# Optimization experiments

Measured on AMD Instinct MI355X. Metric: run time of the kernel, lower is better.

Reference implementation:

```python
import jax, jax.numpy as jnp
import numpy as np

NUM_HEADS = 8
HEAD_DIM = 128
ATTN_SCALE = 0.12


def _rope_tables(T, head_dim, dtype=jnp.float32):
    # half-truncate RoPE from modded-nanogpt: base-freq bounded, half the dims unrotated
    angular_freq = (1.0 / 1024.0) ** jnp.linspace(0.0, 1.0, head_dim // 4, dtype=dtype)
    angular_freq = jnp.concatenate([angular_freq, jnp.zeros(head_dim // 4, dtype=dtype)])  # [D/2]
    t = jnp.arange(T, dtype=dtype)
    theta = t[:, None] * angular_freq[None, :]  # [T, D/2]
    return jnp.cos(theta), jnp.sin(theta)


def _apply_rope(x, cos, sin):
    # x: [B, T, H, D]; cos/sin: [T, D/2]
    x1, x2 = jnp.split(x, 2, axis=-1)
    c = cos[None, :, None, :]
    s = sin[None, :, None, :]
    y1 = x1 * c + x2 * s
    y2 = x2 * c - x1 * s
    return jnp.concatenate([y1, y2], axis=-1)


def _rms_norm(x):
    eps = jnp.asarray(jnp.finfo(x.dtype).eps, x.dtype)
    var = jnp.mean(jnp.square(x), axis=-1, keepdims=True)
    return x * jax.lax.rsqrt(var + eps)


def setup_inputs() -> dict:
    key = jax.random.key(0)
    ks = jax.random.split(key, 4)
    B, T, dim = 1, 4096, 1024
    hdim = NUM_HEADS * HEAD_DIM
    std = 0.5 * dim ** (-0.5)
    bound = (3.0 ** 0.5) * std
    x = jax.random.normal(ks[0], (B, T, dim), dtype=jnp.float32)
    ve = jax.random.normal(ks[1], (B, T, hdim), dtype=jnp.float32)
    qkv_w = jax.random.uniform(ks[2], (3, hdim, dim), dtype=jnp.float32, minval=-bound, maxval=bound)
    lambdas = jnp.array([0.5, 0.5], dtype=jnp.float32)
    c_proj_w = jax.random.normal(ks[3], (dim, hdim), dtype=jnp.float32) * 0.02
    return {"x": x, "ve": ve, "qkv_w": qkv_w, "lambdas": lambdas, "c_proj_w": c_proj_w}


def reference(x, ve, qkv_w, lambdas, c_proj_w):
    B, T, dim = x.shape
    H, D = NUM_HEADS, HEAD_DIM
    # fused QKV projection: qkv_w is [3, H*D, dim]
    w = qkv_w.reshape(3 * H * D, dim)
    qkv = jnp.einsum('btd,fd->btf', x, w).reshape(B, T, 3, H, D)
    q, k, v = qkv[:, :, 0], qkv[:, :, 1], qkv[:, :, 2]  # each [B, T, H, D]
    q = _rms_norm(q)
    k = _rms_norm(k)
    cos, sin = _rope_tables(T, D, dtype=jnp.float32)
    q = _apply_rope(q, cos, sin)
    k = _apply_rope(k, cos, sin)
    # lambda-weighted value blend with value embeddings
    v = lambdas[0] * v + lambdas[1] * ve.reshape(B, T, H, D)
    # causal attention, scale = 0.12
    scores = jnp.einsum('bthd,bshd->bhts', q, k) * ATTN_SCALE  # [B, H, T, T]
    causal = jnp.tril(jnp.ones((T, T), dtype=bool))
    scores = jnp.where(causal[None, None, :, :], scores, jnp.asarray(-jnp.inf, scores.dtype))
    p = jax.nn.softmax(scores, axis=-1)
    y = jnp.einsum('bhts,bshd->bthd', p, v).reshape(B, T, H * D)
    return jnp.einsum('btf,df->btd', y, c_proj_w)
```

## Files before the change

kernel.cpp:

```cpp
#include <hip/hip_runtime.h>
#include <hip/hip_bf16.h>

typedef __attribute__((ext_vector_type(4))) float f32x4;
typedef __attribute__((ext_vector_type(16))) float f32x16;
typedef __attribute__((ext_vector_type(8))) __bf16 bf16x8;
typedef unsigned short u16;
typedef unsigned int u32;
typedef __attribute__((ext_vector_type(4))) u16 u16x4;

__device__ __forceinline__ u16 f2bf(float f) {
    u32 u = __builtin_bit_cast(u32, f);
    u32 r = (u + 0x7FFFu + ((u >> 16) & 1u)) >> 16;
    return (u16)r;
}
__device__ __forceinline__ float bf2f(u16 h) {
    return __builtin_bit_cast(float, ((u32)h) << 16);
}
__device__ __forceinline__ bf16x8 ld_frag(const u16* p) {
    uint4 v = *reinterpret_cast<const uint4*>(p);
    return __builtin_bit_cast(bf16x8, v);
}
__device__ __forceinline__ void gld_lds(const u16* gp, u16* lp) {
    __builtin_amdgcn_global_load_lds(
        (const __attribute__((address_space(1))) u32*)gp,
        (__attribute__((address_space(3))) u32*)lp, 16, 0, 0);
}
__device__ __forceinline__ u32 pk_bf16(float lo, float hi) {
    u32 r;
    asm("v_cvt_pk_bf16_f32 %0, %1, %2" : "=v"(r) : "v"(lo), "v"(hi));
    return r;
}
__device__ __forceinline__ void unp8(uint4 v, float* f) {
    f[0] = bf2f((u16)(v.x & 0xffffu)); f[1] = bf2f((u16)(v.x >> 16));
    f[2] = bf2f((u16)(v.y & 0xffffu)); f[3] = bf2f((u16)(v.y >> 16));
    f[4] = bf2f((u16)(v.z & 0xffffu)); f[5] = bf2f((u16)(v.z >> 16));
    f[6] = bf2f((u16)(v.w & 0xffffu)); f[7] = bf2f((u16)(v.w >> 16));
}

__global__ __launch_bounds__(256) void cvt3(const float* __restrict__ x,
                                            const float* __restrict__ w,
                                            const float* __restrict__ c,
                                            u16* __restrict__ xb,
                                            u16* __restrict__ wb,
                                            u16* __restrict__ cb) {
    int b = blockIdx.x;
    const float* in;
    u16* out;
    int i;
    if (b < 4096)      { in = x; out = xb; i = b * 256 + threadIdx.x; }
    else if (b < 7168) { in = w; out = wb; i = (b - 4096) * 256 + threadIdx.x; }
    else               { in = c; out = cb; i = (b - 7168) * 256 + threadIdx.x; }
    float4 v = reinterpret_cast<const float4*>(in)[i];
    u16x4 o;
    o.x = f2bf(v.x); o.y = f2bf(v.y); o.z = f2bf(v.z); o.w = f2bf(v.w);
    *reinterpret_cast<u16x4*>(out + 4 * (size_t)i) = o;
}

__global__ __launch_bounds__(256) void rope_tab(float* __restrict__ ctab,
                                                float* __restrict__ stab) {
    int i = blockIdx.x * 256 + threadIdx.x;
    int t = i >> 6, j = i & 63;
    float c = 1.0f, s = 0.0f;
    if (j < 32) {
        float f = exp2f(-10.0f * (float)j / 31.0f);
        float th = (float)t * f;
        c = cosf(th); s = sinf(th);
    }
    ctab[i] = c; stab[i] = s;
}

__global__ __launch_bounds__(256, 6) void gemm_qkv(const u16* __restrict__ A,
                                                   const u16* __restrict__ B,
                                                   const float* __restrict__ ve,
                                                   const float* __restrict__ lambdas,
                                                   const float* __restrict__ ctab,
                                                   const float* __restrict__ stab,
                                                   u16* __restrict__ Qb,
                                                   u16* __restrict__ Kb,
                                                   u16* __restrict__ Vt) {
    __shared__ u16 smem[12288];
    const int K = 1024;
    const int tid = threadIdx.x;
    const int w = tid >> 6, l = tid & 63;
    const int bid = blockIdx.x;
    const int bm = bid & 63, bn = bid >> 6;
    const int g = l >> 4, c16 = l & 15;
    const int wr = w >> 1, wc = w & 1;

    f32x4 acc[2][4] = {};

    auto stage = [&](int bi, int kt) {
        {
            int r = w * 16 + (l >> 2);
            int gs = (l & 3) ^ ((r >> 1) & 3);
            gld_lds(A + (size_t)(bm * 64 + r) * K + kt * 32 + gs * 8,
                    smem + bi * 2048 + w * 512);
        }
#pragma unroll
        for (int cc = 0; cc < 2; ++cc) {
            int c = 2 * w + cc;
            int r = 16 * c + (l >> 2);
            int gs = (l & 3) ^ ((r >> 1) & 3);
            gld_lds(B + (size_t)(bn * 128 + r) * K + kt * 32 + gs * 8,
                    smem + 4096 + bi * 4096 + c * 512);
        }
    };

    const int NT = K >> 5;
    stage(0, 0);
    __syncthreads();
    for (int kt = 0; kt < NT; ++kt) {
        int cur = kt & 1;
        if (kt + 1 < NT) stage(cur ^ 1, kt + 1);
        bf16x8 af[2], bf[4];
#pragma unroll
        for (int mi = 0; mi < 2; ++mi) {
            int r = wr * 32 + mi * 16 + c16;
            int sl = g ^ ((r >> 1) & 3);
            af[mi] = ld_frag(smem + cur * 2048 + r * 32 + sl * 8);
        }
#pragma unroll
        for (int ni = 0; ni < 4; ++ni) {
            int r = wc * 64 + ni * 16 + c16;
            int sl = g ^ ((r >> 1) & 3);
            bf[ni] = ld_frag(smem + 4096 + cur * 4096 + r * 32 + sl * 8);
        }
#pragma unroll
        for (int mi = 0; mi < 2; ++mi)
#pragma unroll
            for (int ni = 0; ni < 4; ++ni)
                acc[mi][ni] = __builtin_amdgcn_mfma_f32_16x16x32_bf16(
                    af[mi], bf[ni], acc[mi][ni], 0, 0, 0);
        __syncthreads();
    }

    const int which = bn >> 3, h = bn & 7;
    if (which < 2) {
#pragma unroll
        for (int mi = 0; mi < 2; ++mi)
#pragma unroll
            for (int ni = 0; ni < 4; ++ni) {
                int col = wc * 64 + ni * 16 + c16;
                int row0 = wr * 32 + mi * 16 + g * 4;
#pragma unroll
                for (int r = 0; r < 4; ++r)
                    smem[(row0 + r) * 136 + col] = f2bf(acc[mi][ni][r]);
            }
        __syncthreads();
        const int row = tid >> 2, p = tid & 3;
        const int t = bm * 64 + row;
        const u16* src = smem + row * 136;
        const int j0 = p * 16;
        float x1[16], x2[16];
#pragma unroll
        for (int e = 0; e < 16; e += 8) {
            unp8(*(const uint4*)(src + j0 + e), x1 + e);
            unp8(*(const uint4*)(src + 64 + j0 + e), x2 + e);
        }
        float ss = 0.0f;
#pragma unroll
        for (int e = 0; e < 16; ++e) ss += x1[e] * x1[e] + x2[e] * x2[e];
        ss += __shfl_xor(ss, 1);
        ss += __shfl_xor(ss, 2);
        float rs = rsqrtf(ss * (1.0f / 128.0f) + 1.1920929e-07f);
        if (which == 0) rs *= 0.12f;
        u16* dst = (which ? Kb : Qb) + ((size_t)h * 4096 + t) * 128;
        u16 o1[16], o2[16];
#pragma unroll
        for (int e = 0; e < 16; ++e) {
            int j = j0 + e;
            float c = ctab[t * 64 + j], s = stab[t * 64 + j];
            float a = x1[e] * rs, b = x2[e] * rs;
            o1[e] = f2bf(a * c + b * s);
            o2[e] = f2bf(b * c - a * s);
        }
#pragma unroll
        for (int e = 0; e < 16; e += 4) {
            *(u16x4*)(dst + j0 + e) = *(u16x4*)(o1 + e);
            *(u16x4*)(dst + 64 + j0 + e) = *(u16x4*)(o2 + e);
        }
    } else {
        const float l0 = lambdas[0], l1 = lambdas[1];
#pragma unroll
        for (int mi = 0; mi < 2; ++mi)
#pragma unroll
            for (int ni = 0; ni < 4; ++ni) {
                int col = wc * 64 + ni * 16 + c16;
                int row0 = wr * 32 + mi * 16 + g * 4;
#pragma unroll
                for (int r = 0; r < 4; ++r) {
                    int row = row0 + r;
                    float vv = l0 * acc[mi][ni][r]
                             + l1 * ve[(size_t)(bm * 64 + row) * 1024 + h * 128 + col];
                    int cp = (row & 51) | ((row & 4) << 1) | ((row & 8) >> 1);
                    smem[col * 72 + cp] = f2bf(vv);
                }
            }
        __syncthreads();
        const int d = tid >> 1, seg = tid & 1;
        const u16* lsrc = smem + d * 72 + seg * 32;
        u16* gdst = Vt + ((size_t)h * 128 + d) * 4096 + bm * 64 + seg * 32;
#pragma unroll
        for (int q2 = 0; q2 < 4; ++q2)
            *(uint4*)(gdst + q2 * 8) = *(const uint4*)(lsrc + q2 * 8);
    }
}

__global__ __launch_bounds__(256) void gemm_nt_f32(const u16* __restrict__ A,
                                                   const u16* __restrict__ B,
                                                   float* __restrict__ Cout,
                                                   int M, int N, int K, int ldc) {
    __shared__ u16 smem[8192];
    const int tid = threadIdx.x;
    const int w = tid >> 6, l = tid & 63;
    const int bm = blockIdx.x & 63, bn = blockIdx.x >> 6;
    const int g = l >> 4, c16 = l & 15;
    const int wr = w >> 1, wc = w & 1;

    f32x4 acc[2][2] = {};

    auto stage = [&](int bi, int kt) {
        {
            int r = w * 16 + (l >> 2);
            int gs = (l & 3) ^ ((r >> 1) & 3);
            gld_lds(A + (size_t)(bm * 64 + r) * K + kt * 32 + gs * 8,
                    smem + bi * 2048 + w * 512);
        }
        {
            int r = w * 16 + (l >> 2);
            int gs = (l & 3) ^ ((r >> 1) & 3);
            gld_lds(B + (size_t)(bn * 64 + r) * K + kt * 32 + gs * 8,
                    smem + 4096 + bi * 2048 + w * 512);
        }
    };

    const int NT = K >> 5;
    stage(0, 0);
    __syncthreads();
    for (int kt = 0; kt < NT; ++kt) {
        int cur = kt & 1;
        if (kt + 1 < NT) stage(cur ^ 1, kt + 1);
        bf16x8 af[2], bf[2];
#pragma unroll
        for (int mi = 0; mi < 2; ++mi) {
            int r = wr * 32 + mi * 16 + c16;
            int sl = g ^ ((r >> 1) & 3);
            af[mi] = ld_frag(smem + cur * 2048 + r * 32 + sl * 8);
        }
#pragma unroll
        for (int ni = 0; ni < 2; ++ni) {
            int r = wc * 32 + ni * 16 + c16;
            int sl = g ^ ((r >> 1) & 3);
            bf[ni] = ld_frag(smem + 4096 + cur * 2048 + r * 32 + sl * 8);
        }
#pragma unroll
        for (int mi = 0; mi < 2; ++mi)
#pragma unroll
            for (int ni = 0; ni < 2; ++ni)
                acc[mi][ni] = __builtin_amdgcn_mfma_f32_16x16x32_bf16(
                    af[mi], bf[ni], acc[mi][ni], 0, 0, 0);
        __syncthreads();
    }
#pragma unroll
    for (int mi = 0; mi < 2; ++mi) {
#pragma unroll
        for (int ni = 0; ni < 2; ++ni) {
            int col = bn * 64 + wc * 32 + ni * 16 + c16;
            int row0 = bm * 64 + wr * 32 + mi * 16 + g * 4;
#pragma unroll
            for (int r = 0; r < 4; ++r)
                Cout[(size_t)(row0 + r) * ldc + col] = acc[mi][ni][r];
        }
    }
}

#define OPHALF 4194304
__global__ __launch_bounds__(256) void attn(const u16* __restrict__ Qb,
                                            const u16* __restrict__ Kb,
                                            const u16* __restrict__ Vt,
                                            u16* __restrict__ Op,
                                            float* __restrict__ ssumP) {
    __shared__ u16 smem[3 * 8192];
    const int bid = blockIdx.x;
    const int h = bid & 7;
    const int pid = bid >> 3;
    const int j = pid >> 1;
    const int half = pid & 1;
    const int tid = threadIdx.x;
    const int w = tid >> 6, l = tid & 63;
    const int qh = w & 1, kvh = w >> 1;
    const int l31 = l & 31, hi = l >> 5;
    const int krow = kvh * 32 + l31;

    for (int seg = 0; seg < 2; ++seg) {
        const int qb = seg ? (63 - j) : j;
        const int part = seg ? (1 - half) : half;
        const int s = (qb + 1) >> 1;
        const int t0 = part ? s : 0;
        const int t1 = part ? (qb + 1) : s;
        const int qg = qb * 64 + qh * 32 + l31;

        bf16x8 qf[8];
        {
            const u16* qp = Qb + ((size_t)h * 4096 + qg) * 128;
#pragma unroll
            for (int dk = 0; dk < 8; ++dk) qf[dk] = ld_frag(qp + dk * 16 + hi * 8);
        }

        const u16* kp[4];
        const u16* vp[4];
#pragma unroll
        for (int cc = 0; cc < 4; ++cc) {
            int c = 4 * w + cc;
            int rK = 4 * c + (l >> 4);
            int gsK = (l & 15) ^ (rK & 7);
            kp[cc] = Kb + ((size_t)h * 4096 + t0 * 64 + rK) * 128 + gsK * 8;
            int rV = 8 * c + (l >> 3);
            int gsV = (l & 7) ^ (rV & 7);
            vp[cc] = Vt + ((size_t)h * 128 + rV) * 4096 + t0 * 64 + gsV * 8;
        }

        f32x16 o[4] = {};
        float ssum = 0.0f;

        if (t0 < t1) {
#pragma unroll
            for (int cc = 0; cc < 4; ++cc) {
                gld_lds(kp[cc], smem + (4 * w + cc) * 512);
                kp[cc] += 8192;
            }
            __syncthreads();

            int cur = 0;
            for (int t = t0; t < t1; ++t) {
                if (t + 1 < t1) {
#pragma unroll
                    for (int cc = 0; cc < 4; ++cc) {
                        gld_lds(kp[cc], smem + (cur ^ 1) * 8192 + (4 * w + cc) * 512);
                        kp[cc] += 8192;
                    }
                }
#pragma unroll
                for (int cc = 0; cc < 4; ++cc) {
                    gld_lds(vp[cc], smem + 16384 + (4 * w + cc) * 512);
                    vp[cc] += 64;
                }

                const u16* sKc = smem + cur * 8192;
                f32x16 st = {};
                __builtin_amdgcn_s_setprio(1);
#pragma unroll
                for (int dk = 0; dk < 8; ++dk) {
                    int sl = (2 * dk + hi) ^ (krow & 7);
                    bf16x8 kf = ld_frag(sKc + krow * 128 + sl * 8);
                    st = __builtin_amdgcn_mfma_f32_32x32x16_bf16(kf, qf[dk], st, 0, 0, 0);
                }
                __builtin_amdgcn_s_setprio(0);

                float pv[16];
                if (t == qb) {
#pragma unroll
                    for (int r = 0; r < 16; ++r) {
                        int kvg = t * 64 + kvh * 32 + (r & 3) + 8 * (r >> 2) + 4 * hi;
                        pv[r] = (kvg <= qg) ? __expf(st[r]) : 0.0f;
                    }
                } else {
#pragma unroll
                    for (int r = 0; r < 16; ++r) pv[r] = __expf(st[r]);
                }
                float ps = 0.0f;
#pragma unroll
                for (int i = 0; i < 16; ++i) ps += pv[i];
                ssum += ps;

                bf16x8 pb[2];
#pragma unroll
                for (int m = 0; m < 2; ++m) {
                    uint4 u;
                    u.x = pk_bf16(pv[8 * m + 0], pv[8 * m + 1]);
                    u.y = pk_bf16(pv[8 * m + 2], pv[8 * m + 3]);
                    u.z = pk_bf16(pv[8 * m + 4], pv[8 * m + 5]);
                    u.w = pk_bf16(pv[8 * m + 6], pv[8 * m + 7]);
                    pb[m] = __builtin_bit_cast(bf16x8, u);
                }

                __syncthreads();

                const u16* sVc = smem + 16384;
                __builtin_amdgcn_s_setprio(1);
#pragma unroll
                for (int m = 0; m < 2; ++m) {
#pragma unroll
                    for (int dt = 0; dt < 4; ++dt) {
                        int drow = dt * 32 + l31;
                        int sl = (4 * kvh + 2 * m + hi) ^ (drow & 7);
                        bf16x8 vf = ld_frag(sVc + drow * 64 + sl * 8);
                        o[dt] = __builtin_amdgcn_mfma_f32_32x32x16_bf16(vf, pb[m], o[dt], 0, 0, 0);
                    }
                }
                __builtin_amdgcn_s_setprio(0);
                __syncthreads();
                cur ^= 1;
            }
        } else {
            __syncthreads();
        }

        ssum += __shfl_xor(ssum, 32);

        float* sO = (float*)smem;
        float* sS = (float*)smem + 8448;
        if (kvh == 1) {
            float* base = sO + (qh * 32 + l31) * 132;
#pragma unroll
            for (int dt = 0; dt < 4; ++dt)
#pragma unroll
                for (int i = 0; i < 4; ++i) {
                    int d0 = dt * 32 + i * 8 + hi * 4;
                    float4 v = {o[dt][4 * i + 0], o[dt][4 * i + 1],
                                o[dt][4 * i + 2], o[dt][4 * i + 3]};
                    *(float4*)(base + d0) = v;
                }
            if (hi == 0) sS[qh * 32 + l31] = ssum;
        }
        __syncthreads();
        if (kvh == 0) {
            float stot = ssum + sS[qh * 32 + l31];
            const float* base = sO + (qh * 32 + l31) * 132;
            u16* orow = Op + (size_t)part * OPHALF + ((size_t)(h * 4096 + qg)) * 128;
#pragma unroll
            for (int dt = 0; dt < 4; ++dt)
#pragma unroll
                for (int i = 0; i < 4; ++i) {
                    int d0 = dt * 32 + i * 8 + hi * 4;
                    float4 prev = *(const float4*)(base + d0);
                    u16x4 ov;
                    ov.x = f2bf(o[dt][4 * i + 0] + prev.x);
                    ov.y = f2bf(o[dt][4 * i + 1] + prev.y);
                    ov.z = f2bf(o[dt][4 * i + 2] + prev.z);
                    ov.w = f2bf(o[dt][4 * i + 3] + prev.w);
                    *(u16x4*)(orow + d0) = ov;
                }
            if (hi == 0) ssumP[part * 32768 + h * 4096 + qg] = stot;
        }
        __syncthreads();
    }
}

__global__ __launch_bounds__(256) void combine(const u16* __restrict__ Op,
                                               const float* __restrict__ ssumP,
                                               u16* __restrict__ Y) {
    int i = blockIdx.x * 256 + threadIdx.x;
    int d4 = i & 31;
    int hq = i >> 5;
    int h = hq >> 12, q = hq & 4095;
    u16x4 a = ((const u16x4*)Op)[i];
    u16x4 b = ((const u16x4*)(Op + OPHALF))[i];
    float inv = 1.0f / (ssumP[hq] + ssumP[32768 + hq]);
    u16x4 ov;
    ov.x = f2bf((bf2f(a.x) + bf2f(b.x)) * inv);
    ov.y = f2bf((bf2f(a.y) + bf2f(b.y)) * inv);
    ov.z = f2bf((bf2f(a.z) + bf2f(b.z)) * inv);
    ov.w = f2bf((bf2f(a.w) + bf2f(b.w)) * inv);
    *(u16x4*)(Y + (size_t)q * 1024 + h * 128 + d4 * 4) = ov;
}

extern "C" void kernel_launch(void* const* d_in, const int* in_sizes, int n_in,
                              void* d_out, int out_size, void* d_ws, size_t ws_size,
                              hipStream_t stream) {
    const float* x = (const float*)d_in[0];
    const float* ve = (const float*)d_in[1];
    const float* qkv_w = (const float*)d_in[2];
    const float* lambdas = (const float*)d_in[3];
    const float* c_proj_w = (const float*)d_in[4];

    char* ws = (char*)d_ws;
    size_t o = 0;
    u16* qkvb = (u16*)(ws + o); o += (size_t)4096 * 3072 * 2;
    u16* xb   = (u16*)(ws + o); o += (size_t)4096 * 1024 * 2;
    u16* wb   = (u16*)(ws + o); o += (size_t)3072 * 1024 * 2;
    u16* cb   = (u16*)(ws + o); o += (size_t)1024 * 1024 * 2;
    u16* Qb   = (u16*)(ws + o); o += (size_t)8 * 4096 * 128 * 2;
    u16* Kb   = (u16*)(ws + o); o += (size_t)8 * 4096 * 128 * 2;
    u16* Vt   = (u16*)(ws + o); o += (size_t)8 * 4096 * 128 * 2;
    u16* Yb   = (u16*)(ws + o); o += (size_t)4096 * 1024 * 2;
    float* ctab = (float*)(ws + o); o += (size_t)4096 * 64 * 4;
    float* stab = (float*)(ws + o); o += (size_t)4096 * 64 * 4;
    u16* Op      = qkvb;
    float* ssumP = (float*)wb;

    cvt3<<<8192, 256, 0, stream>>>(x, qkv_w, c_proj_w, xb, wb, cb);
    rope_tab<<<1024, 256, 0, stream>>>(ctab, stab);
    gemm_qkv<<<64 * 24, 256, 0, stream>>>(xb, wb, ve, lambdas, ctab, stab, Qb, Kb, Vt);
    attn<<<512, 256, 0, stream>>>(Qb, Kb, Vt, Op, ssumP);
    combine<<<4096, 256, 0, stream>>>(Op, ssumP, Yb);
    gemm_nt_f32<<<64 * 16, 256, 0, stream>>>(Yb, cb, (float*)d_out, 4096, 1024, 1024, 1024);
}
```

Measured before the change: 137.3 us.

## Process two 64-row query blocks per attention block to reuse K/V tiles

Each attention workgroup now handles a 128-row query tile as two 64-row sub-tiles that share every K and V tile loaded into LDS. This halves global-to-LDS K/V traffic and barrier count per query row, and roughly doubles MFMA work per sync. The causal work split is rebalanced to 32 query tiles with a new midpoint split, and the kernel gets a launch-bounds occupancy hint of 2. It costs many more registers (two Q fragment sets, two score and output accumulators), which may limit occupancy. The grid launch is presumably changed outside the shown lines.

```diff
diff --git a/kernel.cpp b/kernel.cpp
--- a/kernel.cpp
+++ b/kernel.cpp
@@ -275,11 +275,11 @@
 }
 
 #define OPHALF 4194304
-__global__ __launch_bounds__(256) void attn(const u16* __restrict__ Qb,
-                                            const u16* __restrict__ Kb,
-                                            const u16* __restrict__ Vt,
-                                            u16* __restrict__ Op,
-                                            float* __restrict__ ssumP) {
+__global__ __launch_bounds__(256, 2) void attn(const u16* __restrict__ Qb,
+                                               const u16* __restrict__ Kb,
+                                               const u16* __restrict__ Vt,
+                                               u16* __restrict__ Op,
+                                               float* __restrict__ ssumP) {
     __shared__ u16 smem[3 * 8192];
     const int bid = blockIdx.x;
     const int h = bid & 7;
@@ -293,157 +293,168 @@
     const int krow = kvh * 32 + l31;
 
     for (int seg = 0; seg < 2; ++seg) {
-        const int qb = seg ? (63 - j) : j;
+        const int qb = seg ? (31 - j) : j;
         const int part = seg ? (1 - half) : half;
-        const int s = (qb + 1) >> 1;
+        const int s = qb + 1;
         const int t0 = part ? s : 0;
-        const int t1 = part ? (qb + 1) : s;
-        const int qg = qb * 64 + qh * 32 + l31;
-
-        bf16x8 qf[8];
-        {
-            const u16* qp = Qb + ((size_t)h * 4096 + qg) * 128;
-#pragma unroll
-            for (int dk = 0; dk < 8; ++dk) qf[dk] = ld_frag(qp + dk * 16 + hi * 8);
+        const int t1 = part ? (2 * qb + 2) : s;
+        const int qg0 = qb * 128 + qh * 32 + l31;
+        const int qg1 = qg0 + 64;
+
+        bf16x8 qf[2][8];
+#pragma unroll
+        for (int u = 0; u < 2; ++u) {
+            const u16* qp = Qb + ((size_t)h * 4096 + (u ? qg1 : qg0)) * 128;
+#pragma unroll
+            for (int dk = 0; dk < 8; ++dk) qf[u][dk] = ld_frag(qp + dk * 16 + hi * 8);
         }
 
         const u16* kp[4];
-        const u16* vp[4];
+        const u16* vp0;
 #pragma unroll
         for (int cc = 0; cc < 4; ++cc) {
             int c = 4 * w + cc;
             int rK = 4 * c + (l >> 4);
             int gsK = (l & 15) ^ (rK & 7);
             kp[cc] = Kb + ((size_t)h * 4096 + t0 * 64 + rK) * 128 + gsK * 8;
-            int rV = 8 * c + (l >> 3);
-            int gsV = (l & 7) ^ (rV & 7);
-            vp[cc] = Vt + ((size_t)h * 128 + rV) * 4096 + t0 * 64 + gsV * 8;
-        }
-
-        f32x16 o[4] = {};
-        float ssum = 0.0f;
-
-        if (t0 < t1) {
-#pragma unroll
-            for (int cc = 0; cc < 4; ++cc) {
-                gld_lds(kp[cc], smem + (4 * w + cc) * 512);
-                kp[cc] += 8192;
-            }
-            __syncthreads();
-
-            int cur = 0;
-            for (int t = t0; t < t1; ++t) {
-                if (t + 1 < t1) {
-#pragma unroll
-                    for (int cc = 0; cc < 4; ++cc) {
-                        gld_lds(kp[cc], smem + (cur ^ 1) * 8192 + (4 * w + cc) * 512);
-                        kp[cc] += 8192;
-                    }
+        }
+        {
+            int rV = 8 * (4 * w) + (l >> 3);
+            int gsV = (l & 7) ^ ((l >> 3) & 7);
+            vp0 = Vt + ((size_t)h * 128 + rV) * 4096 + t0 * 64 + gsV * 8;
+        }
+
+        f32x16 o[2][4] = {};
+        float ssum[2] = {0.0f, 0.0f};
+
+#pragma unroll
+        for (int cc = 0; cc < 4; ++cc) {
+            gld_lds(kp[cc], smem + (4 * w + cc) * 512);
+            kp[cc] += 8192;
+        }
+        __syncthreads();
+
+        int cur = 0;
+        for (int t = t0; t < t1; ++t) {
+            if (t + 1 < t1) {
+#pragma unroll
+                for (int cc = 0; cc < 4; ++cc) {
+                    gld_lds(kp[cc], smem + (cur ^ 1) * 8192 + (4 * w + cc) * 512);
+                    kp[cc] += 8192;
                 }
-#pragma unroll
-                for (int cc = 0; cc < 4; ++cc) {
-                    gld_lds(vp[cc], smem + 16384 + (4 * w + cc) * 512);
-                    vp[cc] += 64;
-                }
-
-                const u16* sKc = smem + cur * 8192;
-                f32x16 st = {};
-                __builtin_amdgcn_s_setprio(1);
-#pragma unroll
-                for (int dk = 0; dk < 8; ++dk) {
-                    int sl = (2 * dk + hi) ^ (krow & 7);
-                    bf16x8 kf = ld_frag(sKc + krow * 128 + sl * 8);
-                    st = __builtin_amdgcn_mfma_f32_32x32x16_bf16(kf, qf[dk], st, 0, 0, 0);
-                }
-                __builtin_amdgcn_s_setprio(0);
-
+            }
+#pragma unroll
+            for (int cc = 0; cc < 4; ++cc)
+                gld_lds(vp0 + (size_t)cc * 8 * 4096, smem + 16384 + (4 * w + cc) * 512);
+            vp0 += 64;
+
+            const u16* sKc = smem + cur * 8192;
+            f32x16 st0 = {}, st1 = {};
+            __builtin_amdgcn_s_setprio(1);
+#pragma unroll
+            for (int dk = 0; dk < 8; ++dk) {
+                int sl = (2 * dk + hi) ^ (krow & 7);
+                bf16x8 kf = ld_frag(sKc + krow * 128 + sl * 8);
+                st0 = __builtin_amdgcn_mfma_f32_32x32x16_bf16(kf, qf[0][dk], st0, 0, 0, 0);
+                st1 = __builtin_amdgcn_mfma_f32_32x32x16_bf16(kf, qf[1][dk], st1, 0, 0, 0);
+            }
+            __builtin_amdgcn_s_setprio(0);
+
+            bf16x8 pb[2][2];
+#pragma unroll
+            for (int u = 0; u < 2; ++u) {
+                f32x16 stv = u ? st1 : st0;
+                const int qg = u ? qg1 : qg0;
+                const int qmin = qb * 128 + u * 64 + qh * 32;
                 float pv[16];
-                if (t == qb) {
+                if (t * 64 + 63 > qmin) {
 #pragma unroll
                     for (int r = 0; r < 16; ++r) {
                         int kvg = t * 64 + kvh * 32 + (r & 3) + 8 * (r >> 2) + 4 * hi;
-                        pv[r] = (kvg <= qg) ? __expf(st[r]) : 0.0f;
+                        pv[r] = (kvg <= qg) ? __expf(stv[r]) : 0.0f;
                     }
                 } else {
 #pragma unroll
-                    for (int r = 0; r < 16; ++r) pv[r] = __expf(st[r]);
+                    for (int r = 0; r < 16; ++r) pv[r] = __expf(stv[r]);
                 }
                 float ps = 0.0f;
 #pragma unroll
                 for (int i = 0; i < 16; ++i) ps += pv[i];
-                ssum += ps;
-
-                bf16x8 pb[2];
+                ssum[u] += ps;
 #pragma unroll
                 for (int m = 0; m < 2; ++m) {
-                    uint4 u;
-                    u.x = pk_bf16(pv[8 * m + 0], pv[8 * m + 1]);
-                    u.y = pk_bf16(pv[8 * m + 2], pv[8 * m + 3]);
-                    u.z = pk_bf16(pv[8 * m + 4], pv[8 * m + 5]);
-                    u.w = pk_bf16(pv[8 * m + 6], pv[8 * m + 7]);
-                    pb[m] = __builtin_bit_cast(bf16x8, u);
+                    uint4 uu;
+                    uu.x = pk_bf16(pv[8 * m + 0], pv[8 * m + 1]);
+                    uu.y = pk_bf16(pv[8 * m + 2], pv[8 * m + 3]);
+                    uu.z = pk_bf16(pv[8 * m + 4], pv[8 * m + 5]);
+                    uu.w = pk_bf16(pv[8 * m + 6], pv[8 * m + 7]);
+                    pb[u][m] = __builtin_bit_cast(bf16x8, uu);
                 }
-
-                __syncthreads();
-
-                const u16* sVc = smem + 16384;
-                __builtin_amdgcn_s_setprio(1);
-#pragma unroll
-                for (int m = 0; m < 2; ++m) {
-#pragma unroll
-                    for (int dt = 0; dt < 4; ++dt) {
-                        int drow = dt * 32 + l31;
-                        int sl = (4 * kvh + 2 * m + hi) ^ (drow & 7);
-                        bf16x8 vf = ld_frag(sVc + drow * 64 + sl * 8);
-                        o[dt] = __builtin_amdgcn_mfma_f32_32x32x16_bf16(vf, pb[m], o[dt], 0, 0, 0);
-                    }
+            }
+
+            __syncthreads();
+
+            const u16* sVc = smem + 16384;
+            __builtin_amdgcn_s_setprio(1);
+#pragma unroll
+            for (int m = 0; m < 2; ++m) {
+#pragma unroll
+                for (int dt = 0; dt < 4; ++dt) {
+                    int drow = dt * 32 + l31;
+                    int sl = (4 * kvh + 2 * m + hi) ^ (drow & 7);
+                    bf16x8 vf = ld_frag(sVc + drow * 64 + sl * 8);
+                    o[0][dt] = __builtin_amdgcn_mfma_f32_32x32x16_bf16(vf, pb[0][m], o[0][dt], 0, 0, 0);
+                    o[1][dt] = __builtin_amdgcn_mfma_f32_32x32x16_bf16(vf, pb[1][m], o[1][dt], 0, 0, 0);
                 }
-                __builtin_amdgcn_s_setprio(0);
-                __syncthreads();
-                cur ^= 1;
-            }
-        } else {
+            }
+            __builtin_amdgcn_s_setprio(0);
             __syncthreads();
-        }
-
-        ssum += __shfl_xor(ssum, 32);
+            cur ^= 1;
+        }
+
+        ssum[0] += __shfl_xor(ssum[0], 32);
+        ssum[1] += __shfl_xor(ssum[1], 32);
 
         float* sO = (float*)smem;
         float* sS = (float*)smem + 8448;
-        if (kvh == 1) {
-            float* base = sO + (qh * 32 + l31) * 132;
-#pragma unroll
-            for (int dt = 0; dt < 4; ++dt)
-#pragma unroll
-                for (int i = 0; i < 4; ++i) {
-                    int d0 = dt * 32 + i * 8 + hi * 4;
-                    float4 v = {o[dt][4 * i + 0], o[dt][4 * i + 1],
-                                o[dt][4 * i + 2], o[dt][4 * i + 3]};
-                    *(float4*)(base + d0) = v;
-                }
-            if (hi == 0) sS[qh * 32 + l31] = ssum;
-        }
-        __syncthreads();
-        if (kvh == 0) {
-            float stot = ssum + sS[qh * 32 + l31];
-            const float* base = sO + (qh * 32 + l31) * 132;
-            u16* orow = Op + (size_t)part * OPHALF + ((size_t)(h * 4096 + qg)) * 128;
-#pragma unroll
-            for (int dt = 0; dt < 4; ++dt)
-#pragma unroll
-                for (int i = 0; i < 4; ++i) {
-                    int d0 = dt * 32 + i * 8 + hi * 4;
-                    float4 prev = *(const float4*)(base + d0);
-                    u16x4 ov;
-                    ov.x = f2bf(o[dt][4 * i + 0] + prev.x);
-                    ov.y = f2bf(o[dt][4 * i + 1] + prev.y);
-                    ov.z = f2bf(o[dt][4 * i + 2] + prev.z);
-                    ov.w = f2bf(o[dt][4 * i + 3] + prev.w);
-                    *(u16x4*)(orow + d0) = ov;
-                }
-            if (hi == 0) ssumP[part * 32768 + h * 4096 + qg] = stot;
-        }
-        __syncthreads();
+#pragma unroll
+        for (int p = 0; p < 2; ++p) {
+            if (kvh == 1) {
+                float* base = sO + (qh * 32 + l31) * 132;
+#pragma unroll
+                for (int dt = 0; dt < 4; ++dt)
+#pragma unroll
+                    for (int i = 0; i < 4; ++i) {
+                        int d0 = dt * 32 + i * 8 + hi * 4;
+                        float4 v = {o[p][dt][4 * i + 0], o[p][dt][4 * i + 1],
+                                    o[p][dt][4 * i + 2], o[p][dt][4 * i + 3]};
+                        *(float4*)(base + d0) = v;
+                    }
+                if (hi == 0) sS[qh * 32 + l31] = ssum[p];
+            }
+            __syncthreads();
+            if (kvh == 0) {
+                float stot = ssum[p] + sS[qh * 32 + l31];
+                const float* base = sO + (qh * 32 + l31) * 132;
+                int qg = qb * 128 + p * 64 + qh * 32 + l31;
+                u16* orow = Op + (size_t)part * OPHALF + ((size_t)(h * 4096 + qg)) * 128;
+#pragma unroll
+                for (int dt = 0; dt < 4; ++dt)
+#pragma unroll
+                    for (int i = 0; i < 4; ++i) {
+                        int d0 = dt * 32 + i * 8 + hi * 4;
+                        float4 prev = *(const float4*)(base + d0);
+                        u16x4 ov;
+                        ov.x = f2bf(o[p][dt][4 * i + 0] + prev.x);
+                        ov.y = f2bf(o[p][dt][4 * i + 1] + prev.y);
+                        ov.z = f2bf(o[p][dt][4 * i + 2] + prev.z);
+                        ov.w = f2bf(o[p][dt][4 * i + 3] + prev.w);
+                        *(u16x4*)(orow + d0) = ov;
+                    }
+                if (hi == 0) ssumP[part * 32768 + h * 4096 + qg] = stot;
+            }
+            __syncthreads();
+        }
     }
 }
 
```

After: 218.2 us. 1.59x slower.

## Fuse split-attention combine into output GEMM and merge rope table with conversion

Applied to the files above, without the earlier changes.

The kernel that combines the two split-KV attention partials is folded into the A-operand load of the output projection GEMM. Each tile now loads both partials, sums them, scales by the inverse softmax sum, packs to bf16 and writes to LDS, so the Y intermediate round trip and one launch go away. The RoPE table computation is also merged into the conversion kernel to save another launch. In exchange, the A operand is loaded through registers with ALU work instead of async global-to-LDS loads, and the partial data is reread for every N tile (16 times).

```diff
diff --git a/kernel.cpp b/kernel.cpp
--- a/kernel.cpp
+++ b/kernel.cpp
@@ -8,6 +8,8 @@
 typedef unsigned int u32;
 typedef __attribute__((ext_vector_type(4))) u16 u16x4;
 
+#define OPHALF 4194304
+
 __device__ __forceinline__ u16 f2bf(float f) {
     u32 u = __builtin_bit_cast(u32, f);
     u32 r = (u + 0x7FFFu + ((u >> 16) & 1u)) >> 16;
@@ -37,13 +39,27 @@
     f[6] = bf2f((u16)(v.w & 0xffffu)); f[7] = bf2f((u16)(v.w >> 16));
 }
 
-__global__ __launch_bounds__(256) void cvt3(const float* __restrict__ x,
-                                            const float* __restrict__ w,
-                                            const float* __restrict__ c,
-                                            u16* __restrict__ xb,
-                                            u16* __restrict__ wb,
-                                            u16* __restrict__ cb) {
+__global__ __launch_bounds__(256) void prep0(const float* __restrict__ x,
+                                             const float* __restrict__ w,
+                                             const float* __restrict__ c,
+                                             u16* __restrict__ xb,
+                                             u16* __restrict__ wb,
+                                             u16* __restrict__ cb,
+                                             float* __restrict__ ctab,
+                                             float* __restrict__ stab) {
     int b = blockIdx.x;
+    if (b >= 8192) {
+        int i = (b - 8192) * 256 + threadIdx.x;
+        int t = i >> 6, j = i & 63;
+        float cc = 1.0f, ss = 0.0f;
+        if (j < 32) {
+            float f = exp2f(-10.0f * (float)j / 31.0f);
+            float th = (float)t * f;
+            cc = cosf(th); ss = sinf(th);
+        }
+        ctab[i] = cc; stab[i] = ss;
+        return;
+    }
     const float* in;
     u16* out;
     int i;
@@ -54,19 +70,6 @@
     u16x4 o;
     o.x = f2bf(v.x); o.y = f2bf(v.y); o.z = f2bf(v.z); o.w = f2bf(v.w);
     *reinterpret_cast<u16x4*>(out + 4 * (size_t)i) = o;
-}
-
-__global__ __launch_bounds__(256) void rope_tab(float* __restrict__ ctab,
-                                                float* __restrict__ stab) {
-    int i = blockIdx.x * 256 + threadIdx.x;
-    int t = i >> 6, j = i & 63;
-    float c = 1.0f, s = 0.0f;
-    if (j < 32) {
-        float f = exp2f(-10.0f * (float)j / 31.0f);
-        float th = (float)t * f;
-        c = cosf(th); s = sinf(th);
-    }
-    ctab[i] = c; stab[i] = s;
 }
 
 __global__ __launch_bounds__(256, 6) void gemm_qkv(const u16* __restrict__ A,
@@ -206,75 +209,6 @@
     }
 }
 
-__global__ __launch_bounds__(256) void gemm_nt_f32(const u16* __restrict__ A,
-                                                   const u16* __restrict__ B,
-                                                   float* __restrict__ Cout,
-                                                   int M, int N, int K, int ldc) {
-    __shared__ u16 smem[8192];
-    const int tid = threadIdx.x;
-    const int w = tid >> 6, l = tid & 63;
-    const int bm = blockIdx.x & 63, bn = blockIdx.x >> 6;
-    const int g = l >> 4, c16 = l & 15;
-    const int wr = w >> 1, wc = w & 1;
-
-    f32x4 acc[2][2] = {};
-
-    auto stage = [&](int bi, int kt) {
-        {
-            int r = w * 16 + (l >> 2);
-            int gs = (l & 3) ^ ((r >> 1) & 3);
-            gld_lds(A + (size_t)(bm * 64 + r) * K + kt * 32 + gs * 8,
-                    smem + bi * 2048 + w * 512);
-        }
-        {
-            int r = w * 16 + (l >> 2);
-            int gs = (l & 3) ^ ((r >> 1) & 3);
-            gld_lds(B + (size_t)(bn * 64 + r) * K + kt * 32 + gs * 8,
-                    smem + 4096 + bi * 2048 + w * 512);
-        }
-    };
-
-    const int NT = K >> 5;
-    stage(0, 0);
-    __syncthreads();
-    for (int kt = 0; kt < NT; ++kt) {
-        int cur = kt & 1;
-        if (kt + 1 < NT) stage(cur ^ 1, kt + 1);
-        bf16x8 af[2], bf[2];
-#pragma unroll
-        for (int mi = 0; mi < 2; ++mi) {
-            int r = wr * 32 + mi * 16 + c16;
-            int sl = g ^ ((r >> 1) & 3);
-            af[mi] = ld_frag(smem + cur * 2048 + r * 32 + sl * 8);
-        }
-#pragma unroll
-        for (int ni = 0; ni < 2; ++ni) {
-            int r = wc * 32 + ni * 16 + c16;
-            int sl = g ^ ((r >> 1) & 3);
-            bf[ni] = ld_frag(smem + 4096 + cur * 2048 + r * 32 + sl * 8);
-        }
-#pragma unroll
-        for (int mi = 0; mi < 2; ++mi)
-#pragma unroll
-            for (int ni = 0; ni < 2; ++ni)
-                acc[mi][ni] = __builtin_amdgcn_mfma_f32_16x16x32_bf16(
-                    af[mi], bf[ni], acc[mi][ni], 0, 0, 0);
-        __syncthreads();
-    }
-#pragma unroll
-    for (int mi = 0; mi < 2; ++mi) {
-#pragma unroll
-        for (int ni = 0; ni < 2; ++ni) {
-            int col = bn * 64 + wc * 32 + ni * 16 + c16;
-            int row0 = bm * 64 + wr * 32 + mi * 16 + g * 4;
-#pragma unroll
-            for (int r = 0; r < 4; ++r)
-                Cout[(size_t)(row0 + r) * ldc + col] = acc[mi][ni][r];
-        }
-    }
-}
-
-#define OPHALF 4194304
 __global__ __launch_bounds__(256) void attn(const u16* __restrict__ Qb,
                                             const u16* __restrict__ Kb,
                                             const u16* __restrict__ Vt,
@@ -447,22 +381,99 @@
     }
 }
 
-__global__ __launch_bounds__(256) void combine(const u16* __restrict__ Op,
-                                               const float* __restrict__ ssumP,
-                                               u16* __restrict__ Y) {
-    int i = blockIdx.x * 256 + threadIdx.x;
-    int d4 = i & 31;
-    int hq = i >> 5;
-    int h = hq >> 12, q = hq & 4095;
-    u16x4 a = ((const u16x4*)Op)[i];
-    u16x4 b = ((const u16x4*)(Op + OPHALF))[i];
-    float inv = 1.0f / (ssumP[hq] + ssumP[32768 + hq]);
-    u16x4 ov;
-    ov.x = f2bf((bf2f(a.x) + bf2f(b.x)) * inv);
-    ov.y = f2bf((bf2f(a.y) + bf2f(b.y)) * inv);
-    ov.z = f2bf((bf2f(a.z) + bf2f(b.z)) * inv);
-    ov.w = f2bf((bf2f(a.w) + bf2f(b.w)) * inv);
-    *(u16x4*)(Y + (size_t)q * 1024 + h * 128 + d4 * 4) = ov;
+__global__ __launch_bounds__(256) void gemm_out(const u16* __restrict__ Op,
+                                                const float* __restrict__ ssumP,
+                                                const u16* __restrict__ B,
+                                                float* __restrict__ Cout) {
+    __shared__ u16 smem[8192];
+    const int K = 1024;
+    const int tid = threadIdx.x;
+    const int w = tid >> 6, l = tid & 63;
+    const int bm = blockIdx.x & 63, bn = blockIdx.x >> 6;
+    const int g = l >> 4, c16 = l & 15;
+    const int wr = w >> 1, wc = w & 1;
+    const int rr = w * 16 + (l >> 2);
+    const int R  = bm * 64 + rr;
+    const int gsA = (l & 3) ^ ((rr >> 1) & 3);
+
+    f32x4 acc[2][2] = {};
+
+    auto ldA = [&](int kt, uint4& a, uint4& b2, float& inv) {
+        int h = kt >> 2;
+        int d0 = (kt & 3) * 32 + gsA * 8;
+        const u16* p0 = Op + ((size_t)(h * 4096 + R)) * 128 + d0;
+        a  = *(const uint4*)p0;
+        b2 = *(const uint4*)(p0 + OPHALF);
+        inv = 1.0f / (ssumP[h * 4096 + R] + ssumP[32768 + h * 4096 + R]);
+    };
+    auto wrA = [&](int bi, uint4 a, uint4 b2, float inv) {
+        const u16* pa = (const u16*)&a;
+        const u16* pb = (const u16*)&b2;
+        u32 pk[4];
+#pragma unroll
+        for (int i = 0; i < 4; ++i) {
+            float lo = (bf2f(pa[2 * i])     + bf2f(pb[2 * i]))     * inv;
+            float hi = (bf2f(pa[2 * i + 1]) + bf2f(pb[2 * i + 1])) * inv;
+            pk[i] = pk_bf16(lo, hi);
+        }
+        *(uint4*)(smem + bi * 2048 + rr * 32 + (l & 3) * 8) = *(uint4*)pk;
+    };
+    auto stageB = [&](int bi, int kt) {
+        int r = w * 16 + (l >> 2);
+        int gs = (l & 3) ^ ((r >> 1) & 3);
+        gld_lds(B + (size_t)(bn * 64 + r) * K + kt * 32 + gs * 8,
+                smem + 4096 + bi * 2048 + w * 512);
+    };
+
+    const int NT = K >> 5;
+    {
+        uint4 a0, b0; float inv0;
+        ldA(0, a0, b0, inv0);
+        stageB(0, 0);
+        wrA(0, a0, b0, inv0);
+    }
+    __syncthreads();
+    for (int kt = 0; kt < NT; ++kt) {
+        int cur = kt & 1;
+        uint4 aN, bN; float invN;
+        const bool pre = (kt + 1 < NT);
+        if (pre) {
+            ldA(kt + 1, aN, bN, invN);
+            stageB(cur ^ 1, kt + 1);
+        }
+        bf16x8 af[2], bf[2];
+#pragma unroll
+        for (int mi = 0; mi < 2; ++mi) {
+            int r = wr * 32 + mi * 16 + c16;
+            int sl = g ^ ((r >> 1) & 3);
+            af[mi] = ld_frag(smem + cur * 2048 + r * 32 + sl * 8);
+        }
+#pragma unroll
+        for (int ni = 0; ni < 2; ++ni) {
+            int r = wc * 32 + ni * 16 + c16;
+            int sl = g ^ ((r >> 1) & 3);
+            bf[ni] = ld_frag(smem + 4096 + cur * 2048 + r * 32 + sl * 8);
+        }
+#pragma unroll
+        for (int mi = 0; mi < 2; ++mi)
+#pragma unroll
+            for (int ni = 0; ni < 2; ++ni)
+                acc[mi][ni] = __builtin_amdgcn_mfma_f32_16x16x32_bf16(
+                    af[mi], bf[ni], acc[mi][ni], 0, 0, 0);
+        if (pre) wrA(cur ^ 1, aN, bN, invN);
+        __syncthreads();
+    }
+#pragma unroll
+    for (int mi = 0; mi < 2; ++mi) {
+#pragma unroll
+        for (int ni = 0; ni < 2; ++ni) {
+            int col = bn * 64 + wc * 32 + ni * 16 + c16;
+            int row0 = bm * 64 + wr * 32 + mi * 16 + g * 4;
+#pragma unroll
+            for (int r = 0; r < 4; ++r)
+                Cout[(size_t)(row0 + r) * 1024 + col] = acc[mi][ni][r];
+        }
+    }
 }
 
 extern "C" void kernel_launch(void* const* d_in, const int* in_sizes, int n_in,
@@ -486,13 +497,12 @@
     u16* Yb   = (u16*)(ws + o); o += (size_t)4096 * 1024 * 2;
     float* ctab = (float*)(ws + o); o += (size_t)4096 * 64 * 4;
     float* stab = (float*)(ws + o); o += (size_t)4096 * 64 * 4;
+    (void)Yb;
     u16* Op      = qkvb;
     float* ssumP = (float*)wb;
 
-    cvt3<<<8192, 256, 0, stream>>>(x, qkv_w, c_proj_w, xb, wb, cb);
-    rope_tab<<<1024, 256, 0, stream>>>(ctab, stab);
+    prep0<<<9216, 256, 0, stream>>>(x, qkv_w, c_proj_w, xb, wb, cb, ctab, stab);
     gemm_qkv<<<64 * 24, 256, 0, stream>>>(xb, wb, ve, lambdas, ctab, stab, Qb, Kb, Vt);
     attn<<<512, 256, 0, stream>>>(Qb, Kb, Vt, Op, ssumP);
-    combine<<<4096, 256, 0, stream>>>(Op, ssumP, Yb);
-    gemm_nt_f32<<<64 * 16, 256, 0, stream>>>(Yb, cb, (float*)d_out, 4096, 1024, 1024, 1024);
-}
+    gemm_out<<<64 * 16, 256, 0, stream>>>(Op, ssumP, cb, (float*)d_out);
+}
```

Result: slower. 143.0 us (+4.2%).
